# Optimization experiments

Hardware: AMD Instinct MI355X
Metric: run time of the kernel (lower is better)

Reference implementation:

```python
import jax, jax.numpy as jnp
import numpy as np

EPS = 1e-6

def _layernorm(x, g, b):
    m = jnp.mean(x, axis=-1, keepdims=True)
    v = jnp.var(x, axis=-1, keepdims=True)
    return (x - m) / jnp.sqrt(v + EPS) * g + b

def setup_inputs() -> dict:
    key = jax.random.key(0)
    ks = jax.random.split(key, 12)
    B, L, D, H = 2, 1024, 1024, 16
    s = 0.02  # weight init scale
    return {
        "query": jax.random.normal(ks[0], (B, L, D), jnp.float32),
        "pos_bias": jax.random.normal(ks[1], (H, L, L), jnp.float32) * 0.1,
        "postag_bias": jax.random.normal(ks[2], (B, H, L, L), jnp.float32) * 0.1,
        "lex_mask": jax.random.normal(ks[3], (B, L), jnp.float32) * 0.1,
        "mask": jax.random.randint(ks[4], (B, L), 0, 2).astype(jnp.int32),
        "Wq": jax.random.normal(ks[5], (D, D), jnp.float32) * s,
        "bq": jnp.zeros((D,), jnp.float32),
        "Wk": jax.random.normal(ks[6], (D, D), jnp.float32) * s,
        "bk": jnp.zeros((D,), jnp.float32),
        "Wv": jax.random.normal(ks[7], (D, D), jnp.float32) * s,
        "bv": jnp.zeros((D,), jnp.float32),
        "Wo": jax.random.normal(ks[8], (D, D), jnp.float32) * s,
        "bo": jnp.zeros((D,), jnp.float32),
        "gamma": jnp.ones((D,), jnp.float32),
        "beta": jnp.zeros((D,), jnp.float32),
    }

def reference(query, pos_bias, postag_bias, lex_mask, mask,
              Wq, bq, Wk, bk, Wv, bv, Wo, bo, gamma, beta):
    B, L, D = query.shape
    H = pos_bias.shape[0]
    dk = D // H
    scale = jnp.asarray(dk ** 0.5, query.dtype)

    residual = query
    context = query              # context=None path: set BEFORE pre-LN norm
    qn = _layernorm(query, gamma, beta)  # pre_ln=True applies only to query

    Q = (qn @ Wq.T + bq).reshape(B, L, H, dk)       # bqhd
    K = (context @ Wk.T + bk).reshape(B, L, H, dk)  # bkhd
    V = (context @ Wv.T + bv).reshape(B, L, H, dk)

    # (B,H,L,S) logits with all additive bias terms
    logits = jnp.einsum('bqhd,bkhd->bhqk', Q, K) / scale
    logits = logits + pos_bias[None]               # rel-pos bias (H,L,S)
    logits = logits + postag_bias                  # POS-tag bias (B,H,L,S)
    logits = logits + lex_mask[:, None, None, :]   # additive lexical mask
    logits = jnp.where(mask[:, None, None, :] == 0, -jnp.inf, logits)

    attn = jax.nn.softmax(logits, axis=-1)         # dropout inactive (eval)
    out = jnp.einsum('bhqk,bkhd->bqhd', attn, V).reshape(B, L, D)
    out = out @ Wo.T + bo
    out = out + residual
    return out, attn
```

## Files before the change

### kernel.cpp

```cpp
#include <hip/hip_runtime.h>
#include <hip/hip_bf16.h>
#include <math.h>

constexpr int B = 2, L = 1024, D = 1024, H = 16, DK = 64;
constexpr int M = B * L;
constexpr int DD = D * D;

typedef __attribute__((ext_vector_type(8))) short bf16x8;
typedef __attribute__((ext_vector_type(4))) float f32x4;

__device__ inline unsigned short f2bf(float f) {
    __hip_bfloat16 h = __float2bfloat16(f);
    return __builtin_bit_cast(unsigned short, h);
}

__device__ inline void glds16(const void* g, void* l) {
    __builtin_amdgcn_global_load_lds((const __attribute__((address_space(1))) void*)g,
                                     (__attribute__((address_space(3))) void*)l,
                                     16, 0, 0);
}

__global__ __launch_bounds__(256) void ln2_kernel(const float* __restrict__ x,
                                                  const float* __restrict__ gamma,
                                                  const float* __restrict__ beta,
                                                  unsigned short* __restrict__ qn16,
                                                  unsigned short* __restrict__ q16) {
    int row = blockIdx.x;
    int t = threadIdx.x;
    const float4 v = ((const float4*)(x + (size_t)row * D))[t];
    float s  = v.x + v.y + v.z + v.w;
    float sq = v.x*v.x + v.y*v.y + v.z*v.z + v.w*v.w;
    #pragma unroll
    for (int m = 32; m >= 1; m >>= 1) {
        s  += __shfl_xor(s, m, 64);
        sq += __shfl_xor(sq, m, 64);
    }
    __shared__ float rs[4], rq[4];
    int wid = t >> 6;
    if ((t & 63) == 0) { rs[wid] = s; rq[wid] = sq; }
    __syncthreads();
    s  = rs[0] + rs[1] + rs[2] + rs[3];
    sq = rq[0] + rq[1] + rq[2] + rq[3];
    float mean = s * (1.0f / D);
    float var  = sq * (1.0f / D) - mean * mean;
    float rstd = rsqrtf(var + 1e-6f);
    float4 g  = ((const float4*)gamma)[t];
    float4 bb = ((const float4*)beta)[t];
    ushort4 on, oq;
    on.x = f2bf((v.x - mean) * rstd * g.x + bb.x);
    on.y = f2bf((v.y - mean) * rstd * g.y + bb.y);
    on.z = f2bf((v.z - mean) * rstd * g.z + bb.z);
    on.w = f2bf((v.w - mean) * rstd * g.w + bb.w);
    oq.x = f2bf(v.x); oq.y = f2bf(v.y); oq.z = f2bf(v.z); oq.w = f2bf(v.w);
    ((ushort4*)(qn16 + (size_t)row * D))[t] = on;
    ((ushort4*)(q16  + (size_t)row * D))[t] = oq;
}

__global__ __launch_bounds__(256) void wconv_kernel(const float* __restrict__ Wq,
                                                    const float* __restrict__ Wk,
                                                    const float* __restrict__ Wv,
                                                    const float* __restrict__ Wo,
                                                    unsigned short* __restrict__ out) {
    const float* src = (blockIdx.y == 0) ? Wq : (blockIdx.y == 1) ? Wk
                       : (blockIdx.y == 2) ? Wv : Wo;
    size_t i = (size_t)blockIdx.x * 256 + threadIdx.x;
    float4 v = ((const float4*)src)[i];
    ushort4 o;
    o.x = f2bf(v.x); o.y = f2bf(v.y); o.z = f2bf(v.z); o.w = f2bf(v.w);
    ((ushort4*)(out + (size_t)blockIdx.y * DD))[i] = o;
}

__global__ __launch_bounds__(256) void lsm_kernel(const float* __restrict__ lex,
                                                  const int* __restrict__ mask,
                                                  float* __restrict__ lsm) {
    int i = blockIdx.x * 256 + threadIdx.x;
    lsm[i] = mask[i] ? lex[i] : -1e30f;
}

__global__ __launch_bounds__(256) void gemm_qkv(
        const unsigned short* __restrict__ qn16, const unsigned short* __restrict__ q16,
        const unsigned short* __restrict__ W,
        const float* __restrict__ bq, const float* __restrict__ bk,
        const float* __restrict__ bv,
        unsigned short* __restrict__ Qm, unsigned short* __restrict__ Km,
        unsigned short* __restrict__ Vm) {
    __shared__ __align__(16) unsigned short As[128 * 64];
    __shared__ __align__(16) unsigned short Ws[128 * 64];
    int t = threadIdx.x, lane = t & 63, w = t >> 6;
    int quad = lane >> 4, l15 = lane & 15;
    int nt = blockIdx.x;
    int bm = blockIdx.y * 128;
    const unsigned short* A = (nt < 8) ? qn16 : q16;
    const float* bias = (nt < 8) ? bq : ((nt < 16) ? bk : bv);
    unsigned short* Cout = (nt < 8) ? Qm : ((nt < 16) ? Km : Vm);
    int bn_local = (nt & 7) * 128;
    int wm = (w >> 1) * 64, wn = (w & 1) * 64;
    f32x4 acc[4][4] = {};
    for (int k0 = 0; k0 < D; k0 += 64) {
        __syncthreads();
        const unsigned short* ap = A + (size_t)(bm + w * 32) * D + k0;
        const unsigned short* wp = W + (size_t)(nt * 128 + w * 32) * D + k0;
        #pragma unroll
        for (int i = 0; i < 4; i++) {
            int c = i * 64 + lane;
            int r = c >> 3, g = (c & 7) ^ (r & 7);
            glds16(ap + (size_t)r * D + g * 8, &As[w * 2048 + i * 512]);
            glds16(wp + (size_t)r * D + g * 8, &Ws[w * 2048 + i * 512]);
        }
        __syncthreads();
        #pragma unroll
        for (int k2 = 0; k2 < 2; k2++) {
            bf16x8 av[4], bw[4];
            #pragma unroll
            for (int i = 0; i < 4; i++) {
                int r = wm + i * 16 + l15;
                av[i] = *(const bf16x8*)&As[r * 64 + (((quad + 4 * k2) ^ (r & 7)) * 8)];
            }
            #pragma unroll
            for (int j = 0; j < 4; j++) {
                int r = wn + j * 16 + l15;
                bw[j] = *(const bf16x8*)&Ws[r * 64 + (((quad + 4 * k2) ^ (r & 7)) * 8)];
            }
            #pragma unroll
            for (int i = 0; i < 4; i++)
                #pragma unroll
                for (int j = 0; j < 4; j++)
                    acc[i][j] = __builtin_amdgcn_mfma_f32_16x16x32_bf16(av[i], bw[j], acc[i][j], 0, 0, 0);
        }
    }
    #pragma unroll
    for (int j = 0; j < 4; j++) {
        int col = bn_local + wn + j * 16 + l15;
        float bcol = bias[col];
        #pragma unroll
        for (int i = 0; i < 4; i++)
            #pragma unroll
            for (int rg = 0; rg < 4; rg++) {
                int row = bm + wm + i * 16 + quad * 4 + rg;
                Cout[(size_t)row * D + col] = f2bf(acc[i][j][rg] + bcol);
            }
    }
}

__global__ __launch_bounds__(256) void vtrans_kernel(const unsigned short* __restrict__ Vm,
                                                     unsigned short* __restrict__ Vt) {
    __shared__ unsigned short sb[128 * 66];
    int t = threadIdx.x;
    int z = blockIdx.y;
    int b = z >> 4, h = z & 15;
    int s0 = blockIdx.x * 128;
    size_t base = (size_t)b * L * D + (size_t)h * 64;
    #pragma unroll
    for (int i = 0; i < 4; i++) {
        int idx = t + 256 * i;
        int r = idx >> 3, c8 = idx & 7;
        uint4 vv = *(const uint4*)&Vm[base + (size_t)(s0 + r) * D + c8 * 8];
        unsigned int* sp = (unsigned int*)&sb[r * 66 + c8 * 8];
        sp[0] = vv.x; sp[1] = vv.y; sp[2] = vv.z; sp[3] = vv.w;
    }
    __syncthreads();
    #pragma unroll
    for (int i = 0; i < 4; i++) {
        int idx = t + 256 * i;
        int d = idx >> 4, sc = idx & 15;
        unsigned short tmp[8];
        #pragma unroll
        for (int j = 0; j < 8; j++) tmp[j] = sb[(sc * 8 + j) * 66 + d];
        *(uint4*)&Vt[((size_t)z * 64 + d) * L + s0 + sc * 8] = *(uint4*)tmp;
    }
}

__global__ __launch_bounds__(256, 4) void attn4_kernel(
        const unsigned short* __restrict__ Qm, const unsigned short* __restrict__ Km,
        const float* __restrict__ pos_bias, const float* __restrict__ postag,
        const float* __restrict__ lsm, float* __restrict__ attn_out) {
    __shared__ __align__(16) unsigned short q_sh[16][72];
    __shared__ __align__(16) unsigned short kv_sh[128 * 64];
    __shared__ float lsm_sh[1024];
    __shared__ float redA[16][4], redB[16][4];

    int t = threadIdx.x, lane = t & 63, w = t >> 6;
    int quad = lane >> 4, l15 = lane & 15;
    int qt = blockIdx.x & 63;
    int bh = blockIdx.x >> 6;
    int b = bh >> 4, h = bh & 15;
    int q0 = qt * 16;
    int q = q0 + l15;
    size_t base = (size_t)b * L * D + (size_t)h * DK;

    if (t < 128) {
        int r = t >> 3, c8 = t & 7;
        *(uint4*)&q_sh[r][c8 * 8] = *(const uint4*)&Qm[base + (size_t)(q0 + r) * D + c8 * 8];
    }
    ((float4*)lsm_sh)[t] = ((const float4*)(lsm + b * L))[t];
    __syncthreads();
    bf16x8 qb0 = *(const bf16x8*)&q_sh[l15][quad * 8];
    bf16x8 qb1 = *(const bf16x8*)&q_sh[l15][32 + quad * 8];

    const float* pbp = pos_bias + ((size_t)h * L + q) * L;
    const float* ptp = postag + ((size_t)bh * L + q) * L;

    f32x4 acc[16] = {};
    for (int st = 0; st < 8; st++) {
        __syncthreads();
        const unsigned short* kp = Km + base + (size_t)(st * 128 + w * 32) * D;
        #pragma unroll
        for (int i = 0; i < 4; i++) {
            int c = i * 64 + lane;
            int r = c >> 3, g = (c & 7) ^ (r & 7);
            glds16(kp + (size_t)r * D + g * 8, &kv_sh[w * 2048 + i * 512]);
        }
        int s_u0 = st * 128 + w * 16 + quad * 4;
        int s_u1 = s_u0 + 64;
        float4 pb0 = *(const float4*)(pbp + s_u0);
        float4 pt0 = *(const float4*)(ptp + s_u0);
        float4 pb1 = *(const float4*)(pbp + s_u1);
        float4 pt1 = *(const float4*)(ptp + s_u1);
        __syncthreads();
        #pragma unroll
        for (int u = 0; u < 2; u++) {
            int r = (u * 4 + w) * 16 + l15;
            bf16x8 ka0 = *(const bf16x8*)&kv_sh[r * 64 + ((quad ^ (r & 7)) * 8)];
            bf16x8 ka1 = *(const bf16x8*)&kv_sh[r * 64 + (((quad + 4) ^ (r & 7)) * 8)];
            int ti = 2 * st + u;
            acc[ti] = __builtin_amdgcn_mfma_f32_16x16x32_bf16(ka0, qb0, acc[ti], 0, 0, 0);
            acc[ti] = __builtin_amdgcn_mfma_f32_16x16x32_bf16(ka1, qb1, acc[ti], 0, 0, 0);
        }
        {
            int ti = 2 * st;
            float4 l0 = *(const float4*)&lsm_sh[s_u0];
            acc[ti][0] = acc[ti][0] * 0.125f + (pb0.x + pt0.x + l0.x);
            acc[ti][1] = acc[ti][1] * 0.125f + (pb0.y + pt0.y + l0.y);
            acc[ti][2] = acc[ti][2] * 0.125f + (pb0.z + pt0.z + l0.z);
            acc[ti][3] = acc[ti][3] * 0.125f + (pb0.w + pt0.w + l0.w);
            ti = 2 * st + 1;
            float4 l1 = *(const float4*)&lsm_sh[s_u1];
            acc[ti][0] = acc[ti][0] * 0.125f + (pb1.x + pt1.x + l1.x);
            acc[ti][1] = acc[ti][1] * 0.125f + (pb1.y + pt1.y + l1.y);
            acc[ti][2] = acc[ti][2] * 0.125f + (pb1.z + pt1.z + l1.z);
            acc[ti][3] = acc[ti][3] * 0.125f + (pb1.w + pt1.w + l1.w);
        }
    }
    float mx = -1e30f;
    #pragma unroll
    for (int ti = 0; ti < 16; ti++)
        #pragma unroll
        for (int rg = 0; rg < 4; rg++) mx = fmaxf(mx, acc[ti][rg]);
    mx = fmaxf(mx, __shfl_xor(mx, 16, 64));
    mx = fmaxf(mx, __shfl_xor(mx, 32, 64));
    if (quad == 0) redA[l15][w] = mx;
    __syncthreads();
    mx = fmaxf(fmaxf(redA[l15][0], redA[l15][1]), fmaxf(redA[l15][2], redA[l15][3]));
    float sum = 0.f;
    #pragma unroll
    for (int ti = 0; ti < 16; ti++)
        #pragma unroll
        for (int rg = 0; rg < 4; rg++) {
            float e = __expf(acc[ti][rg] - mx);
            acc[ti][rg] = e;
            sum += e;
        }
    sum += __shfl_xor(sum, 16, 64);
    sum += __shfl_xor(sum, 32, 64);
    if (quad == 0) redB[l15][w] = sum;
    __syncthreads();
    float inv = 1.0f / (redB[l15][0] + redB[l15][1] + redB[l15][2] + redB[l15][3]);
    #pragma unroll
    for (int ti = 0; ti < 16; ti++) {
        int s0 = (ti >> 1) * 128 + (ti & 1) * 64 + w * 16 + quad * 4;
        float4 o;
        o.x = acc[ti][0] * inv; o.y = acc[ti][1] * inv;
        o.z = acc[ti][2] * inv; o.w = acc[ti][3] * inv;
        *(float4*)&attn_out[((size_t)bh * L + q) * L + s0] = o;
    }
}

__global__ __launch_bounds__(256) void gemm_pv(
        const float* __restrict__ attnP, const unsigned short* __restrict__ Vt,
        unsigned short* __restrict__ ctx16) {
    __shared__ __align__(16) unsigned short As[64][72];
    __shared__ __align__(16) unsigned short Ws[64 * 64];
    int t = threadIdx.x, lane = t & 63, w = t >> 6;
    int quad = lane >> 4, l15 = lane & 15;
    int bm = blockIdx.x * 64, z = blockIdx.z;
    int wm = (w >> 1) * 32, wn = (w & 1) * 32;
    int ar = t >> 2, ac = (t & 3) * 16;
    f32x4 acc[2][2] = {};
    for (int k0 = 0; k0 < L; k0 += 64) {
        __syncthreads();
        const unsigned short* wp = Vt + ((size_t)z * 64 + w * 16) * L + k0;
        #pragma unroll
        for (int i = 0; i < 2; i++) {
            int c = i * 64 + lane;
            int r = c >> 3, g = (c & 7) ^ (r & 7);
            glds16(wp + (size_t)r * L + g * 8, &Ws[w * 1024 + i * 512]);
        }
        {
            const float* ap = &attnP[((size_t)z * L + bm + ar) * L + k0 + ac];
            float4 f0 = *(const float4*)ap;
            float4 f1 = *(const float4*)(ap + 4);
            float4 f2 = *(const float4*)(ap + 8);
            float4 f3 = *(const float4*)(ap + 12);
            ushort4 u0, u1, u2, u3;
            u0.x = f2bf(f0.x); u0.y = f2bf(f0.y); u0.z = f2bf(f0.z); u0.w = f2bf(f0.w);
            u1.x = f2bf(f1.x); u1.y = f2bf(f1.y); u1.z = f2bf(f1.z); u1.w = f2bf(f1.w);
            u2.x = f2bf(f2.x); u2.y = f2bf(f2.y); u2.z = f2bf(f2.z); u2.w = f2bf(f2.w);
            u3.x = f2bf(f3.x); u3.y = f2bf(f3.y); u3.z = f2bf(f3.z); u3.w = f2bf(f3.w);
            *(ushort4*)&As[ar][ac]      = u0;
            *(ushort4*)&As[ar][ac + 4]  = u1;
            *(ushort4*)&As[ar][ac + 8]  = u2;
            *(ushort4*)&As[ar][ac + 12] = u3;
        }
        __syncthreads();
        #pragma unroll
        for (int k2 = 0; k2 < 2; k2++) {
            bf16x8 av[2], bw[2];
            #pragma unroll
            for (int i = 0; i < 2; i++)
                av[i] = *(const bf16x8*)&As[wm + i * 16 + l15][k2 * 32 + quad * 8];
            #pragma unroll
            for (int j = 0; j < 2; j++) {
                int r = wn + j * 16 + l15;
                bw[j] = *(const bf16x8*)&Ws[r * 64 + (((quad + 4 * k2) ^ (r & 7)) * 8)];
            }
            #pragma unroll
            for (int i = 0; i < 2; i++)
                #pragma unroll
                for (int j = 0; j < 2; j++)
                    acc[i][j] = __builtin_amdgcn_mfma_f32_16x16x32_bf16(av[i], bw[j], acc[i][j], 0, 0, 0);
        }
    }
    size_t coff = (size_t)(z >> 4) * L * D + (size_t)(z & 15) * 64;
    #pragma unroll
    for (int i = 0; i < 2; i++)
        #pragma unroll
        for (int j = 0; j < 2; j++)
            #pragma unroll
            for (int rg = 0; rg < 4; rg++) {
                int row = bm + wm + i * 16 + quad * 4 + rg;
                int col = wn + j * 16 + l15;
                ctx16[coff + (size_t)row * D + col] = f2bf(acc[i][j][rg]);
            }
}

__global__ __launch_bounds__(256) void gemm_out(
        const unsigned short* __restrict__ A, const unsigned short* __restrict__ W,
        const float* __restrict__ bias, const float* __restrict__ res,
        float* __restrict__ C) {
    __shared__ __align__(16) unsigned short As[64 * 64];
    __shared__ __align__(16) unsigned short Ws[64 * 64];
    int t = threadIdx.x, lane = t & 63, w = t >> 6;
    int quad = lane >> 4, l15 = lane & 15;
    int bm = blockIdx.x * 64, bn = blockIdx.y * 64;
    int wm = (w >> 1) * 32, wn = (w & 1) * 32;
    f32x4 acc[2][2] = {};
    for (int k0 = 0; k0 < D; k0 += 64) {
        __syncthreads();
        const unsigned short* ap = A + (size_t)(bm + w * 16) * D + k0;
        const unsigned short* wp = W + (size_t)(bn + w * 16) * D + k0;
        #pragma unroll
        for (int i = 0; i < 2; i++) {
            int c = i * 64 + lane;
            int r = c >> 3, g = (c & 7) ^ (r & 7);
            glds16(ap + (size_t)r * D + g * 8, &As[w * 1024 + i * 512]);
            glds16(wp + (size_t)r * D + g * 8, &Ws[w * 1024 + i * 512]);
        }
        __syncthreads();
        #pragma unroll
        for (int k2 = 0; k2 < 2; k2++) {
            bf16x8 av[2], bw[2];
            #pragma unroll
            for (int i = 0; i < 2; i++) {
                int r = wm + i * 16 + l15;
                av[i] = *(const bf16x8*)&As[r * 64 + (((quad + 4 * k2) ^ (r & 7)) * 8)];
            }
            #pragma unroll
            for (int j = 0; j < 2; j++) {
                int r = wn + j * 16 + l15;
                bw[j] = *(const bf16x8*)&Ws[r * 64 + (((quad + 4 * k2) ^ (r & 7)) * 8)];
            }
            #pragma unroll
            for (int i = 0; i < 2; i++)
                #pragma unroll
                for (int j = 0; j < 2; j++)
                    acc[i][j] = __builtin_amdgcn_mfma_f32_16x16x32_bf16(av[i], bw[j], acc[i][j], 0, 0, 0);
        }
    }
    #pragma unroll
    for (int j = 0; j < 2; j++) {
        int col = bn + wn + j * 16 + l15;
        float bcol = bias[col];
        #pragma unroll
        for (int i = 0; i < 2; i++)
            #pragma unroll
            for (int rg = 0; rg < 4; rg++) {
                int row = bm + wm + i * 16 + quad * 4 + rg;
                C[(size_t)row * D + col] = acc[i][j][rg] + bcol + res[(size_t)row * D + col];
            }
    }
}

extern "C" void kernel_launch(void* const* d_in, const int* in_sizes, int n_in,
                              void* d_out, int out_size, void* d_ws, size_t ws_size,
                              hipStream_t stream) {
    (void)in_sizes; (void)n_in; (void)out_size; (void)ws_size;
    const float* query  = (const float*)d_in[0];
    const float* pos_b  = (const float*)d_in[1];
    const float* postag = (const float*)d_in[2];
    const float* lex    = (const float*)d_in[3];
    const int*   mask   = (const int*)d_in[4];
    const float* Wq = (const float*)d_in[5];
    const float* bq = (const float*)d_in[6];
    const float* Wk = (const float*)d_in[7];
    const float* bk = (const float*)d_in[8];
    const float* Wv = (const float*)d_in[9];
    const float* bv = (const float*)d_in[10];
    const float* Wo = (const float*)d_in[11];
    const float* bo = (const float*)d_in[12];
    const float* gamma = (const float*)d_in[13];
    const float* beta  = (const float*)d_in[14];

    float* out  = (float*)d_out;
    float* attn = out + (size_t)B * L * D;

    unsigned short* ws16 = (unsigned short*)d_ws;
    const size_t NE = (size_t)M * D;
    unsigned short* qn16  = ws16;
    unsigned short* q16   = ws16 + NE;
    unsigned short* W16   = ws16 + 2 * NE;
    unsigned short* Qm16  = W16 + 4 * (size_t)DD;
    unsigned short* Km16  = Qm16 + NE;
    unsigned short* Vm16  = Km16 + NE;
    unsigned short* Vt16  = Vm16 + NE;
    unsigned short* ctx16 = Vt16 + NE;
    float* lsm = (float*)(ctx16 + NE);

    ln2_kernel<<<M, 256, 0, stream>>>(query, gamma, beta, qn16, q16);
    wconv_kernel<<<dim3(DD / 1024, 4), 256, 0, stream>>>(Wq, Wk, Wv, Wo, W16);
    lsm_kernel<<<M / 256, 256, 0, stream>>>(lex, mask, lsm);
    gemm_qkv<<<dim3(24, 16), 256, 0, stream>>>(qn16, q16, W16, bq, bk, bv,
                                               Qm16, Km16, Vm16);
    vtrans_kernel<<<dim3(8, 32), 256, 0, stream>>>(Vm16, Vt16);
    attn4_kernel<<<B * H * (L / 16), 256, 0, stream>>>(Qm16, Km16, pos_b, postag,
                                                       lsm, attn);
    gemm_pv<<<dim3(16, 1, 32), 256, 0, stream>>>(attn, Vt16, ctx16);
    gemm_out<<<dim3(32, 16), 256, 0, stream>>>(ctx16, W16 + 3 * (size_t)DD, bo, query, out);
}
```

Measured before the change: 418.8 us.

## Fuse P·V product into attention softmax kernel using register-held probabilities

Removes the separate gemm_pv kernel. The attention kernel now converts its normalized probabilities to bf16, stages them in a small LDS tile, and multiplies by transposed V tiles loaded via global_load_lds to produce the context directly. This avoids re-reading the full fp32 attention matrix from global memory. In exchange, each query tile block reloads the whole V slice for its head, adds extra LDS and barriers, and adds serial MFMA work at the tail of the kernel.

After: 408.1 us. 2.6% less time.

```diff
diff --git a/kernel.cpp b/kernel.cpp
--- a/kernel.cpp
+++ b/kernel.cpp
@@ -170,12 +170,15 @@
     }
 }
 
-__global__ __launch_bounds__(256, 4) void attn4_kernel(
+__global__ __launch_bounds__(256, 4) void attn_pv_kernel(
         const unsigned short* __restrict__ Qm, const unsigned short* __restrict__ Km,
+        const unsigned short* __restrict__ Vt,
         const float* __restrict__ pos_bias, const float* __restrict__ postag,
-        const float* __restrict__ lsm, float* __restrict__ attn_out) {
+        const float* __restrict__ lsm, float* __restrict__ attn_out,
+        unsigned short* __restrict__ ctx16) {
     __shared__ __align__(16) unsigned short q_sh[16][72];
     __shared__ __align__(16) unsigned short kv_sh[128 * 64];
+    __shared__ __align__(16) unsigned short p_sh[16][136];
     __shared__ float lsm_sh[1024];
     __shared__ float redA[16][4], redB[16][4];
 
@@ -271,76 +274,39 @@
         float4 o;
         o.x = acc[ti][0] * inv; o.y = acc[ti][1] * inv;
         o.z = acc[ti][2] * inv; o.w = acc[ti][3] * inv;
+        acc[ti][0] = o.x; acc[ti][1] = o.y; acc[ti][2] = o.z; acc[ti][3] = o.w;
         *(float4*)&attn_out[((size_t)bh * L + q) * L + s0] = o;
     }
-}
-
-__global__ __launch_bounds__(256) void gemm_pv(
-        const float* __restrict__ attnP, const unsigned short* __restrict__ Vt,
-        unsigned short* __restrict__ ctx16) {
-    __shared__ __align__(16) unsigned short As[64][72];
-    __shared__ __align__(16) unsigned short Ws[64 * 64];
-    int t = threadIdx.x, lane = t & 63, w = t >> 6;
-    int quad = lane >> 4, l15 = lane & 15;
-    int bm = blockIdx.x * 64, z = blockIdx.z;
-    int wm = (w >> 1) * 32, wn = (w & 1) * 32;
-    int ar = t >> 2, ac = (t & 3) * 16;
-    f32x4 acc[2][2] = {};
-    for (int k0 = 0; k0 < L; k0 += 64) {
-        __syncthreads();
-        const unsigned short* wp = Vt + ((size_t)z * 64 + w * 16) * L + k0;
-        #pragma unroll
-        for (int i = 0; i < 2; i++) {
-            int c = i * 64 + lane;
-            int r = c >> 3, g = (c & 7) ^ (r & 7);
-            glds16(wp + (size_t)r * L + g * 8, &Ws[w * 1024 + i * 512]);
-        }
-        {
-            const float* ap = &attnP[((size_t)z * L + bm + ar) * L + k0 + ac];
-            float4 f0 = *(const float4*)ap;
-            float4 f1 = *(const float4*)(ap + 4);
-            float4 f2 = *(const float4*)(ap + 8);
-            float4 f3 = *(const float4*)(ap + 12);
-            ushort4 u0, u1, u2, u3;
-            u0.x = f2bf(f0.x); u0.y = f2bf(f0.y); u0.z = f2bf(f0.z); u0.w = f2bf(f0.w);
-            u1.x = f2bf(f1.x); u1.y = f2bf(f1.y); u1.z = f2bf(f1.z); u1.w = f2bf(f1.w);
-            u2.x = f2bf(f2.x); u2.y = f2bf(f2.y); u2.z = f2bf(f2.z); u2.w = f2bf(f2.w);
-            u3.x = f2bf(f3.x); u3.y = f2bf(f3.y); u3.z = f2bf(f3.z); u3.w = f2bf(f3.w);
-            *(ushort4*)&As[ar][ac]      = u0;
-            *(ushort4*)&As[ar][ac + 4]  = u1;
-            *(ushort4*)&As[ar][ac + 8]  = u2;
-            *(ushort4*)&As[ar][ac + 12] = u3;
-        }
-        __syncthreads();
-        #pragma unroll
-        for (int k2 = 0; k2 < 2; k2++) {
-            bf16x8 av[2], bw[2];
-            #pragma unroll
-            for (int i = 0; i < 2; i++)
-                av[i] = *(const bf16x8*)&As[wm + i * 16 + l15][k2 * 32 + quad * 8];
-            #pragma unroll
-            for (int j = 0; j < 2; j++) {
-                int r = wn + j * 16 + l15;
-                bw[j] = *(const bf16x8*)&Ws[r * 64 + (((quad + 4 * k2) ^ (r & 7)) * 8)];
-            }
-            #pragma unroll
-            for (int i = 0; i < 2; i++)
-                #pragma unroll
-                for (int j = 0; j < 2; j++)
-                    acc[i][j] = __builtin_amdgcn_mfma_f32_16x16x32_bf16(av[i], bw[j], acc[i][j], 0, 0, 0);
-        }
-    }
-    size_t coff = (size_t)(z >> 4) * L * D + (size_t)(z & 15) * 64;
-    #pragma unroll
-    for (int i = 0; i < 2; i++)
-        #pragma unroll
-        for (int j = 0; j < 2; j++)
-            #pragma unroll
-            for (int rg = 0; rg < 4; rg++) {
-                int row = bm + wm + i * 16 + quad * 4 + rg;
-                int col = wn + j * 16 + l15;
-                ctx16[coff + (size_t)row * D + col] = f2bf(acc[i][j][rg]);
-            }
+    f32x4 cacc = {};
+    const unsigned short* vp = Vt + (size_t)bh * 64 * L;
+    for (int st = 0; st < 8; st++) {
+        __syncthreads();
+        #pragma unroll
+        for (int i = 0; i < 4; i++) {
+            int r = w * 16 + i * 4 + (lane >> 4);
+            int g = (lane & 15) ^ (r & 7);
+            glds16(vp + (size_t)r * L + st * 128 + g * 8, &kv_sh[w * 2048 + i * 512]);
+        }
+        #pragma unroll
+        for (int u = 0; u < 2; u++) {
+            f32x4 p = acc[2 * st + u];
+            ushort4 pu;
+            pu.x = f2bf(p[0]); pu.y = f2bf(p[1]); pu.z = f2bf(p[2]); pu.w = f2bf(p[3]);
+            *(ushort4*)&p_sh[l15][u * 64 + w * 16 + quad * 4] = pu;
+        }
+        __syncthreads();
+        int rv = w * 16 + l15;
+        #pragma unroll
+        for (int kk = 0; kk < 4; kk++) {
+            bf16x8 vf = *(const bf16x8*)&kv_sh[rv * 128 + (((kk * 4 + quad) ^ (rv & 7)) * 8)];
+            bf16x8 pf = *(const bf16x8*)&p_sh[l15][kk * 32 + quad * 8];
+            cacc = __builtin_amdgcn_mfma_f32_16x16x32_bf16(pf, vf, cacc, 0, 0, 0);
+        }
+    }
+    size_t cbase = ((size_t)b * L + q0) * D + (size_t)h * 64 + w * 16 + l15;
+    #pragma unroll
+    for (int rg = 0; rg < 4; rg++)
+        ctx16[cbase + (size_t)(quad * 4 + rg) * D] = f2bf(cacc[rg]);
 }
 
 __global__ __launch_bounds__(256) void gemm_out(
@@ -441,8 +407,8 @@
     gemm_qkv<<<dim3(24, 16), 256, 0, stream>>>(qn16, q16, W16, bq, bk, bv,
                                                Qm16, Km16, Vm16);
     vtrans_kernel<<<dim3(8, 32), 256, 0, stream>>>(Vm16, Vt16);
-    attn4_kernel<<<B * H * (L / 16), 256, 0, stream>>>(Qm16, Km16, pos_b, postag,
-                                                       lsm, attn);
-    gemm_pv<<<dim3(16, 1, 32), 256, 0, stream>>>(attn, Vt16, ctx16);
+    attn_pv_kernel<<<B * H * (L / 16), 256, 0, stream>>>(Qm16, Km16, Vt16,
+                                                         pos_b, postag, lsm,
+                                                         attn, ctx16);
     gemm_out<<<dim3(32, 16), 256, 0, stream>>>(ctx16, W16 + 3 * (size_t)DD, bo, query, out);
 }
```
